# Kernel tuning notes

Measured on AMD Instinct MI355X. Metric: run time of the kernel, lower is better.

The kernel has to match this reference:

```python
import jax, jax.numpy as jnp
import numpy as np

N, D, S, E, H, L = 20000, 256, 4, 320000, 5, 3
EPS = 1e-5


def _layer_norm(x, g, b):
    m = x.mean(-1, keepdims=True)
    v = ((x - m) ** 2).mean(-1, keepdims=True)
    return (x - m) * jax.lax.rsqrt(v + EPS) * g + b


def _gcn_conv(h, src, dst, w, W, b):
    # GCNConv with symmetric normalization and added self-loops (weight 1).
    loops = jnp.arange(N, dtype=src.dtype)
    s = jnp.concatenate([src, loops])
    t = jnp.concatenate([dst, loops])
    we = jnp.concatenate([w, jnp.ones((N,), h.dtype)])
    deg = jax.ops.segment_sum(we, t, num_segments=N)
    dinv = jnp.where(deg > 0, jax.lax.rsqrt(jnp.maximum(deg, EPS)), 0.0)
    norm = dinv[s] * we * dinv[t]          # [E+N]
    hW = h @ W                              # [N, D]
    msg = norm[:, None] * hW[s]             # [E+N, D] gather
    return jax.ops.segment_sum(msg, t, num_segments=N) + b  # scatter-add


def _gelu(x):
    return jax.nn.gelu(x, approximate=False)  # torch nn.GELU default (exact)


def setup_inputs() -> dict:
    key = jax.random.key(0)
    ks = jax.random.split(key, 24)
    f32 = jnp.float32
    w = lambda k, sh, s=0.05: jax.random.normal(k, sh, f32) * s
    inp = {
        "x": jax.random.normal(ks[0], (S, N, D), f32),
        "edge_src": jax.random.randint(ks[1], (E,), 0, N, jnp.int32),
        "edge_dst": jax.random.randint(ks[2], (E,), 0, N, jnp.int32),
        "edge_weight": jax.random.uniform(ks[3], (E,), f32),
        # 3 GCNConv(d, d) layers
        "gcn_W": w(ks[4], (L, D, D)),
        "gcn_b": jnp.zeros((L, D), f32),
        # 3 LayerNorm(d)
        "ln_g": jnp.ones((L, D), f32),
        "ln_b": jnp.zeros((L, D), f32),
        # nn.GRU(d, d) single layer, batch_first
        "gru_Wih": w(ks[5], (3 * D, D)),
        "gru_Whh": w(ks[6], (3 * D, D)),
        "gru_bih": jnp.zeros((3 * D,), f32),
        "gru_bhh": jnp.zeros((3 * D,), f32),
        # ForecastHead: d -> d/2 -> d/4 -> H
        "fc1_W": w(ks[7], (D // 2, D)), "fc1_b": jnp.zeros((D // 2,), f32),
        "fc2_W": w(ks[8], (D // 4, D // 2)), "fc2_b": jnp.zeros((D // 4,), f32),
        "fc3_W": w(ks[9], (H, D // 4)), "fc3_b": jnp.zeros((H,), f32),
        # DirectionHead: d -> d/4 -> H
        "dh1_W": w(ks[10], (D // 4, D)), "dh1_b": jnp.zeros((D // 4,), f32),
        "dh2_W": w(ks[11], (H, D // 4)), "dh2_b": jnp.zeros((H,), f32),
    }
    return inp


def reference(x, edge_src, edge_dst, edge_weight, gcn_W, gcn_b, ln_g, ln_b,
              gru_Wih, gru_Whh, gru_bih, gru_bhh,
              fc1_W, fc1_b, fc2_W, fc2_b, fc3_W, fc3_b,
              dh1_W, dh1_b, dh2_W, dh2_b):
    # Per-snapshot GCN stack (dropout = identity in eval). Loop over the
    # small fixed snapshot count to bound the gather/scatter intermediate.
    feats = []
    for si in range(S):
        h = x[si]
        for l in range(L):
            h = _gcn_conv(h, edge_src, edge_dst, edge_weight, gcn_W[l], gcn_b[l])
            h = _layer_norm(h, ln_g[l], ln_b[l])
            h = jax.nn.relu(h)
        feats.append(h)
    seq = jnp.stack(feats, axis=0)  # [S, N, D] (time-major for scan)

    def gru_step(h, x_t):
        gi = x_t @ gru_Wih.T + gru_bih
        gh = h @ gru_Whh.T + gru_bhh
        ir, iz, ig = jnp.split(gi, 3, axis=-1)
        hr, hz, hg = jnp.split(gh, 3, axis=-1)
        r = jax.nn.sigmoid(ir + hr)
        z = jax.nn.sigmoid(iz + hz)
        n = jnp.tanh(ig + r * hg)
        return (1.0 - z) * n + z * h, None

    h_last, _ = jax.lax.scan(gru_step, jnp.zeros((N, D), x.dtype), seq)

    f = _gelu(h_last @ fc1_W.T + fc1_b)
    f = _gelu(f @ fc2_W.T + fc2_b)
    forecast = f @ fc3_W.T + fc3_b            # [N, H]
    d = _gelu(h_last @ dh1_W.T + dh1_b)
    direction = d @ dh2_W.T + dh2_b           # [N, H]
    return forecast, direction
```

## Files before the change

kernel.cpp:

```cpp
#include <hip/hip_runtime.h>
#include <hip/hip_bf16.h>

constexpr int Nn = 20000;
constexpr int D  = 256;
constexpr int S  = 4;
constexpr int E  = 320000;
constexpr int H  = 5;
constexpr int L  = 3;

using bf16 = __hip_bfloat16;
typedef __attribute__((ext_vector_type(8))) short v8s;
typedef __attribute__((ext_vector_type(4))) float v4f;

#define GLOBAL_AS __attribute__((address_space(1)))
#define LDS_AS    __attribute__((address_space(3)))

__device__ __forceinline__ float gelu_exact(float x) {
    return 0.5f * x * (1.0f + erff(x * 0.70710678118654752440f));
}
__device__ __forceinline__ unsigned short f2bu(float f) {
    bf16 h = __float2bfloat16(f);
    return *reinterpret_cast<unsigned short*>(&h);
}
__device__ __forceinline__ float b2f(unsigned short u) {
    unsigned int v = (unsigned int)u << 16;
    return __uint_as_float(v);
}

__global__ void init_deg_cnt_kernel(float* deg, int* cnt, int n) {
    int i = blockIdx.x * blockDim.x + threadIdx.x;
    if (i < n) { deg[i] = 1.0f; cnt[i] = 0; }
}
__global__ void deg_hist_kernel(const int* __restrict__ dst, const float* __restrict__ w,
                                float* __restrict__ deg, int* __restrict__ cnt, int e) {
    int i = blockIdx.x * blockDim.x + threadIdx.x;
    if (i < e) {
        int d = dst[i];
        atomicAdd(&deg[d], w[i]);
        atomicAdd(&cnt[d], 1);
    }
}
__global__ void dinv_kernel(const float* __restrict__ deg, float* __restrict__ dinv,
                            float* __restrict__ selfnorm, int n) {
    int i = blockIdx.x * blockDim.x + threadIdx.x;
    if (i < n) {
        float dg = deg[i];
        float dv = dg > 0.0f ? rsqrtf(fmaxf(dg, 1e-5f)) : 0.0f;
        dinv[i] = dv;
        selfnorm[i] = dv * dv;
    }
}
__global__ __launch_bounds__(1024) void scan_rowptr_kernel(int* __restrict__ cnt,
                                                           int* __restrict__ rowptr, int n) {
    __shared__ int wsum[16];
    __shared__ int woff[16];
    int t = threadIdx.x;
    int wave = t >> 6, lane = t & 63;
    int chunk = (n + 1023) / 1024;
    int start = t * chunk;
    int end = start + chunk; if (end > n) end = n;
    int s = 0;
    for (int i = start; i < end; ++i) s += cnt[i];
    int incl = s;
#pragma unroll
    for (int off = 1; off < 64; off <<= 1) {
        int v = __shfl_up(incl, off);
        if (lane >= off) incl += v;
    }
    int excl = incl - s;
    if (lane == 63) wsum[wave] = incl;
    __syncthreads();
    if (t == 0) {
        int acc = 0;
        for (int i = 0; i < 16; ++i) { woff[i] = acc; acc += wsum[i]; }
        rowptr[n] = acc;
    }
    __syncthreads();
    int acc = woff[wave] + excl;
    for (int i = start; i < end; ++i) {
        rowptr[i] = acc; acc += cnt[i]; cnt[i] = 0;
    }
}
__global__ void csr_fill_kernel(const int* __restrict__ src, const int* __restrict__ dst,
                                const float* __restrict__ w, const float* __restrict__ dinv,
                                const int* __restrict__ rowptr,
                                int* __restrict__ cursor, int* __restrict__ csrc,
                                float* __restrict__ cnorm, int e) {
    int i = blockIdx.x * blockDim.x + threadIdx.x;
    if (i < e) {
        int sN = src[i], dN = dst[i];
        int pos = rowptr[dN] + atomicAdd(&cursor[dN], 1);
        csrc[pos] = sN;
        cnorm[pos] = dinv[sN] * w[i] * dinv[dN];
    }
}
constexpr int CW0 = L * D * D;
constexpr int CW1 = CW0 + 3 * D * D;
constexpr int CW2 = CW1 + 3 * D * D;
constexpr int CW3 = CW2 + 192 * 256;
constexpr int CW4 = CW3 + 64 * 128;
constexpr int CW5 = CW4 + 4 * D;
constexpr int CW6 = CW5 + 192;
__global__ void convert_weights_kernel(
    const float* __restrict__ gcn_W, const float* __restrict__ Wih,
    const float* __restrict__ Whh, const float* __restrict__ fc1W,
    const float* __restrict__ fc2W, const float* __restrict__ dh1W,
    const float* __restrict__ bih, const float* __restrict__ bhh,
    const float* __restrict__ fc1b, const float* __restrict__ dh1b,
    unsigned short* __restrict__ Wtb, unsigned short* __restrict__ Wihb,
    unsigned short* __restrict__ Whhb, unsigned short* __restrict__ fc1dh1Wb,
    unsigned short* __restrict__ fc2Wb,
    float* __restrict__ gbias, float* __restrict__ hcat)
{
    int i = blockIdx.x * blockDim.x + threadIdx.x;
    if (i < CW0) {
        int l = i / (D * D);
        int rem = i - l * D * D;
        int k = rem / D;
        int n = rem - k * D;
        Wtb[(size_t)l * D * D + (size_t)n * D + k] = f2bu(gcn_W[i]);
    } else if (i < CW1) { int j = i - CW0; Wihb[j] = f2bu(Wih[j]); }
    else if (i < CW2)   { int j = i - CW1; Whhb[j] = f2bu(Whh[j]); }
    else if (i < CW3) {
        int j = i - CW2;
        fc1dh1Wb[j] = (j < 128 * 256) ? f2bu(fc1W[j]) : f2bu(dh1W[j - 128 * 256]);
    }
    else if (i < CW4)   { int j = i - CW3; fc2Wb[j] = f2bu(fc2W[j]); }
    else if (i < CW5) {
        int j = i - CW4;
        int g = j >> 8, d = j & 255;
        float v;
        if (g == 0)      v = bih[d] + bhh[d];
        else if (g == 1) v = bih[D + d] + bhh[D + d];
        else if (g == 2) v = bih[2 * D + d];
        else             v = bhh[2 * D + d];
        gbias[j] = v;
    }
    else if (i < CW6) {
        int j = i - CW5;
        hcat[j] = (j < 128) ? fc1b[j] : dh1b[j - 128];
    }
}

#define GBM 128
#define GBN 128
#define GBK 64
template<int OUT_MODE, int ACT, int XIN>
__global__ __launch_bounds__(256) void gemm_bt_bf16_kernel(
    const unsigned short* __restrict__ A, int lda,
    const unsigned short* __restrict__ B,
    const float* __restrict__ bias, unsigned short* __restrict__ C,
    int M, int N, int K)
{
    __shared__ short As[GBM * GBK];
    __shared__ short Bs[GBN * GBK];
    int tid = threadIdx.x;
    int wave = tid >> 6, lane = tid & 63;
    int ln = lane & 15, quad = lane >> 4;
    int wr = wave >> 1, wc = wave & 1;
    int bm = blockIdx.y * GBM, bn = blockIdx.x * GBN;

    v4f acc[4][4];
#pragma unroll
    for (int i = 0; i < 4; ++i)
#pragma unroll
        for (int j = 0; j < 4; ++j)
            acc[i][j] = (v4f)(0.0f);

    int lrow = lane >> 3;
    int lcol = (lane & 7) * 8;

    for (int k0 = 0; k0 < K; k0 += GBK) {
#pragma unroll
        for (int c = 0; c < 4; ++c) {
            int seg = wave * 4 + c;
            int row = seg * 8 + lrow;
            int gm = bm + row; if (gm >= M) gm = M - 1;
            if (XIN) {
                int xr = (gm & 3) * Nn + (gm >> 2);
                const float* xp = (const float*)A + (size_t)xr * D + k0 + lcol;
                float4 v0 = *(const float4*)xp;
                float4 v1 = *(const float4*)(xp + 4);
                v8s o;
                o[0] = (short)f2bu(v0.x); o[1] = (short)f2bu(v0.y);
                o[2] = (short)f2bu(v0.z); o[3] = (short)f2bu(v0.w);
                o[4] = (short)f2bu(v1.x); o[5] = (short)f2bu(v1.y);
                o[6] = (short)f2bu(v1.z); o[7] = (short)f2bu(v1.w);
                *(v8s*)(&As[row * GBK + lcol]) = o;
            } else {
                __builtin_amdgcn_global_load_lds(
                    (const GLOBAL_AS unsigned int*)(A + (size_t)gm * lda + k0 + lcol),
                    (LDS_AS unsigned int*)(&As[row * GBK + lcol]), 16, 0, 0);
            }
            int gn = bn + row; if (gn >= N) gn = N - 1;
            __builtin_amdgcn_global_load_lds(
                (const GLOBAL_AS unsigned int*)(B + (size_t)gn * K + k0 + lcol),
                (LDS_AS unsigned int*)(&Bs[row * GBK + lcol]), 16, 0, 0);
        }
        __syncthreads();
#pragma unroll
        for (int ks = 0; ks < 2; ++ks) {
            v8s af[4], bfr[4];
#pragma unroll
            for (int i = 0; i < 4; ++i) {
                int row = wr * 64 + i * 16 + ln;
                af[i] = *(const v8s*)(&As[row * GBK + ks * 32 + quad * 8]);
            }
#pragma unroll
            for (int j = 0; j < 4; ++j) {
                int row = wc * 64 + j * 16 + ln;
                bfr[j] = *(const v8s*)(&Bs[row * GBK + ks * 32 + quad * 8]);
            }
#pragma unroll
            for (int i = 0; i < 4; ++i)
#pragma unroll
                for (int j = 0; j < 4; ++j)
                    acc[i][j] = __builtin_amdgcn_mfma_f32_16x16x32_bf16(af[i], bfr[j], acc[i][j], 0, 0, 0);
        }
        __syncthreads();
    }
#pragma unroll
    for (int i = 0; i < 4; ++i) {
        int gmb = bm + wr * 64 + i * 16 + quad * 4;
#pragma unroll
        for (int j = 0; j < 4; ++j) {
            int gn = bn + wc * 64 + j * 16 + ln;
            float bv = (bias && gn < N) ? bias[gn] : 0.0f;
            if (OUT_MODE == 2) {
                ushort4 u;
                u.x = f2bu(acc[i][j][0] + bv);
                u.y = f2bu(acc[i][j][1] + bv);
                u.z = f2bu(acc[i][j][2] + bv);
                u.w = f2bu(acc[i][j][3] + bv);
                int node = gmb >> 2;
                *(ushort4*)(C + ((size_t)node * D + gn) * 4) = u;
            } else {
                if (gn < N) {
#pragma unroll
                    for (int r = 0; r < 4; ++r) {
                        int gm = gmb + r;
                        if (gm < M) {
                            float v = acc[i][j][r] + bv;
                            if (ACT == 1) v = gelu_exact(v);
                            C[(size_t)gm * N + gn] = f2bu(v);
                        }
                    }
                }
            }
        }
    }
}

__global__ __launch_bounds__(256) void gru_fused_kernel(
    const unsigned short* __restrict__ feat, int fstride,
    const unsigned short* __restrict__ hbf,
    const unsigned short* __restrict__ Wihb,
    const unsigned short* __restrict__ Whhb,
    const float* __restrict__ gbias,
    float* __restrict__ h, unsigned short* __restrict__ hb,
    int write_f32, int first)
{
    __shared__ short As[64 * 64];
    __shared__ short Bs[192 * 64];
    int tid = threadIdx.x;
    int wave = tid >> 6, lane = tid & 63;
    int ln = lane & 15, quad = lane >> 4;
    int wm = wave >> 1, wn = wave & 1;
    int bm = blockIdx.y * 64;
    int bn = blockIdx.x * 64;

    v4f accR[2][2], accZ[2][2], accG[2][2], accHG[2][2];
#pragma unroll
    for (int mi = 0; mi < 2; ++mi)
#pragma unroll
        for (int nj = 0; nj < 2; ++nj) {
            accR[mi][nj] = (v4f)(0.0f); accZ[mi][nj] = (v4f)(0.0f);
            accG[mi][nj] = (v4f)(0.0f); accHG[mi][nj] = (v4f)(0.0f);
        }

    int lrow = lane >> 3, lcol = (lane & 7) * 8;
    int nphase = first ? 1 : 2;

    for (int phase = 0; phase < nphase; ++phase) {
        const unsigned short* A = phase ? hbf : feat;
        int astr = phase ? D : fstride;
        const unsigned short* W = phase ? Whhb : Wihb;
        for (int k0 = 0; k0 < D; k0 += 64) {
#pragma unroll
            for (int c = 0; c < 2; ++c) {
                int row = wave * 16 + c * 8 + lrow;
                int gm = bm + row; if (gm >= Nn) gm = Nn - 1;
                __builtin_amdgcn_global_load_lds(
                    (const GLOBAL_AS unsigned int*)(A + (size_t)gm * astr + k0 + lcol),
                    (LDS_AS unsigned int*)(&As[row * 64 + lcol]), 16, 0, 0);
            }
#pragma unroll
            for (int c = 0; c < 6; ++c) {
                int row = wave * 48 + c * 8 + lrow;
                int g = row >> 6, dloc = row & 63;
                __builtin_amdgcn_global_load_lds(
                    (const GLOBAL_AS unsigned int*)(W + ((size_t)(g * D + bn + dloc)) * D + k0 + lcol),
                    (LDS_AS unsigned int*)(&Bs[row * 64 + lcol]), 16, 0, 0);
            }
            __syncthreads();
#pragma unroll
            for (int ks = 0; ks < 2; ++ks) {
                v8s am[2];
#pragma unroll
                for (int mi = 0; mi < 2; ++mi)
                    am[mi] = *(const v8s*)(&As[(wm * 32 + mi * 16 + ln) * 64 + ks * 32 + quad * 8]);
#pragma unroll
                for (int g = 0; g < 3; ++g) {
#pragma unroll
                    for (int nj = 0; nj < 2; ++nj) {
                        v8s bf = *(const v8s*)(&Bs[(g * 64 + wn * 32 + nj * 16 + ln) * 64 + ks * 32 + quad * 8]);
#pragma unroll
                        for (int mi = 0; mi < 2; ++mi) {
                            if (g == 0)
                                accR[mi][nj] = __builtin_amdgcn_mfma_f32_16x16x32_bf16(am[mi], bf, accR[mi][nj], 0, 0, 0);
                            else if (g == 1)
                                accZ[mi][nj] = __builtin_amdgcn_mfma_f32_16x16x32_bf16(am[mi], bf, accZ[mi][nj], 0, 0, 0);
                            else if (phase == 0)
                                accG[mi][nj] = __builtin_amdgcn_mfma_f32_16x16x32_bf16(am[mi], bf, accG[mi][nj], 0, 0, 0);
                            else
                                accHG[mi][nj] = __builtin_amdgcn_mfma_f32_16x16x32_bf16(am[mi], bf, accHG[mi][nj], 0, 0, 0);
                        }
                    }
                }
            }
            __syncthreads();
        }
    }
#pragma unroll
    for (int mi = 0; mi < 2; ++mi) {
        int gm0 = bm + wm * 32 + mi * 16 + quad * 4;
#pragma unroll
        for (int nj = 0; nj < 2; ++nj) {
            int gn = bn + wn * 32 + nj * 16 + ln;
            float vbr = gbias[gn], vbz = gbias[D + gn];
            float vbig = gbias[2 * D + gn], vbhg = gbias[3 * D + gn];
#pragma unroll
            for (int r = 0; r < 4; ++r) {
                int gm = gm0 + r;
                if (gm < Nn) {
                    float rv = 1.0f / (1.0f + expf(-(accR[mi][nj][r] + vbr)));
                    float zv = 1.0f / (1.0f + expf(-(accZ[mi][nj][r] + vbz)));
                    float nv = tanhf(accG[mi][nj][r] + vbig + rv * (accHG[mi][nj][r] + vbhg));
                    float hold = first ? 0.0f : h[(size_t)gm * D + gn];
                    float hv = (1.0f - zv) * nv + zv * hold;
                    if (write_f32) h[(size_t)gm * D + gn] = hv;
                    hb[(size_t)gm * D + gn] = f2bu(hv);
                }
            }
        }
    }
}

__global__ __launch_bounds__(256) void gcn_agg_ln_relu4_kernel(
    const unsigned short* __restrict__ hWb, const int* __restrict__ rowptr,
    const int* __restrict__ csrc, const float* __restrict__ cnorm,
    const float* __restrict__ selfnorm,
    const float* __restrict__ gcn_b, const float* __restrict__ ln_g,
    const float* __restrict__ ln_b, unsigned short* __restrict__ out)
{
    int wave = threadIdx.x >> 6, lane = threadIdx.x & 63;
    int i = blockIdx.x * 4 + wave;
    const ushort4* tbl = (const ushort4*)hWb;

    float acc[4][4];
    {
        float w = selfnorm[i];
#pragma unroll
        for (int q = 0; q < 4; ++q) {
            ushort4 u = tbl[(size_t)i * D + lane + q * 64];
            acc[q][0] = w * b2f(u.x); acc[q][1] = w * b2f(u.y);
            acc[q][2] = w * b2f(u.z); acc[q][3] = w * b2f(u.w);
        }
    }
    int beg = rowptr[i], end = rowptr[i + 1];
    int p = beg;
    for (; p + 1 < end; p += 2) {
        int sA = csrc[p], sB = csrc[p + 1];
        float wA = cnorm[p], wB = cnorm[p + 1];
        ushort4 uA[4], uB[4];
#pragma unroll
        for (int q = 0; q < 4; ++q) uA[q] = tbl[(size_t)sA * D + lane + q * 64];
#pragma unroll
        for (int q = 0; q < 4; ++q) uB[q] = tbl[(size_t)sB * D + lane + q * 64];
#pragma unroll
        for (int q = 0; q < 4; ++q) {
            acc[q][0] = fmaf(wA, b2f(uA[q].x), acc[q][0]);
            acc[q][1] = fmaf(wA, b2f(uA[q].y), acc[q][1]);
            acc[q][2] = fmaf(wA, b2f(uA[q].z), acc[q][2]);
            acc[q][3] = fmaf(wA, b2f(uA[q].w), acc[q][3]);
            acc[q][0] = fmaf(wB, b2f(uB[q].x), acc[q][0]);
            acc[q][1] = fmaf(wB, b2f(uB[q].y), acc[q][1]);
            acc[q][2] = fmaf(wB, b2f(uB[q].z), acc[q][2]);
            acc[q][3] = fmaf(wB, b2f(uB[q].w), acc[q][3]);
        }
    }
    if (p < end) {
        int sA = csrc[p]; float wA = cnorm[p];
#pragma unroll
        for (int q = 0; q < 4; ++q) {
            ushort4 u = tbl[(size_t)sA * D + lane + q * 64];
            acc[q][0] = fmaf(wA, b2f(u.x), acc[q][0]);
            acc[q][1] = fmaf(wA, b2f(u.y), acc[q][1]);
            acc[q][2] = fmaf(wA, b2f(u.z), acc[q][2]);
            acc[q][3] = fmaf(wA, b2f(u.w), acc[q][3]);
        }
    }
#pragma unroll
    for (int q = 0; q < 4; ++q) {
        float bb = gcn_b[lane + q * 64];
        acc[q][0] += bb; acc[q][1] += bb; acc[q][2] += bb; acc[q][3] += bb;
    }
    float s1[4], s2[4];
#pragma unroll
    for (int s = 0; s < 4; ++s) {
        s1[s] = acc[0][s] + acc[1][s] + acc[2][s] + acc[3][s];
        s2[s] = acc[0][s] * acc[0][s] + acc[1][s] * acc[1][s]
              + acc[2][s] * acc[2][s] + acc[3][s] * acc[3][s];
    }
#pragma unroll
    for (int off = 32; off > 0; off >>= 1) {
#pragma unroll
        for (int s = 0; s < 4; ++s) {
            s1[s] += __shfl_xor(s1[s], off);
            s2[s] += __shfl_xor(s2[s], off);
        }
    }
    const float inv = 1.0f / D;
    float m[4], rr[4];
#pragma unroll
    for (int s = 0; s < 4; ++s) {
        m[s] = s1[s] * inv;
        rr[s] = rsqrtf(s2[s] * inv - m[s] * m[s] + 1e-5f);
    }
    size_t ob = (size_t)(i << 2) * D;
#pragma unroll
    for (int q = 0; q < 4; ++q) {
        int d = lane + q * 64;
        float g = ln_g[d], lb = ln_b[d];
#pragma unroll
        for (int s = 0; s < 4; ++s) {
            float y = (acc[q][s] - m[s]) * rr[s] * g + lb;
            out[ob + (size_t)s * D + d] = f2bu(fmaxf(y, 0.0f));
        }
    }
}

__global__ void head5_bf_kernel(const unsigned short* __restrict__ A, int lda,
                                const float* __restrict__ W,
                                const float* __restrict__ b, float* __restrict__ C,
                                int M, int K) {
    int idx = blockIdx.x * blockDim.x + threadIdx.x;
    if (idx >= M * H) return;
    int m = idx / H;
    int h = idx - m * H;
    const ushort4* ar = (const ushort4*)(A + (size_t)m * lda);
    const float* wr = W + (size_t)h * K;
    float s = 0.0f;
    for (int k4 = 0; k4 < K / 4; ++k4) {
        ushort4 u = ar[k4];
        s = fmaf(b2f(u.x), wr[4 * k4 + 0], s);
        s = fmaf(b2f(u.y), wr[4 * k4 + 1], s);
        s = fmaf(b2f(u.z), wr[4 * k4 + 2], s);
        s = fmaf(b2f(u.w), wr[4 * k4 + 3], s);
    }
    C[idx] = s + b[h];
}

extern "C" void kernel_launch(void* const* d_in, const int* in_sizes, int n_in,
                              void* d_out, int out_size, void* d_ws, size_t ws_size,
                              hipStream_t stream)
{
    const float* x     = (const float*)d_in[0];
    const int*   esrc  = (const int*)d_in[1];
    const int*   edst  = (const int*)d_in[2];
    const float* ew    = (const float*)d_in[3];
    const float* gcn_W = (const float*)d_in[4];
    const float* gcn_b = (const float*)d_in[5];
    const float* ln_g  = (const float*)d_in[6];
    const float* ln_b  = (const float*)d_in[7];
    const float* Wih   = (const float*)d_in[8];
    const float* Whh   = (const float*)d_in[9];
    const float* bih   = (const float*)d_in[10];
    const float* bhh   = (const float*)d_in[11];
    const float* fc1W  = (const float*)d_in[12];
    const float* fc1b  = (const float*)d_in[13];
    const float* fc2W  = (const float*)d_in[14];
    const float* fc2b  = (const float*)d_in[15];
    const float* fc3W  = (const float*)d_in[16];
    const float* fc3b  = (const float*)d_in[17];
    const float* dh1W  = (const float*)d_in[18];
    const float* dh1b  = (const float*)d_in[19];
    const float* dh2W  = (const float*)d_in[20];
    const float* dh2b  = (const float*)d_in[21];

    float* out = (float*)d_out;

    char* p = (char*)d_ws;
    auto alloc = [&](size_t bytes) -> void* {
        void* r = (void*)p;
        p += (bytes + 255) & ~(size_t)255;
        return r;
    };
    float* deg      = (float*)alloc((size_t)Nn * 4);
    float* dinv     = (float*)alloc((size_t)Nn * 4);
    float* selfnorm = (float*)alloc((size_t)Nn * 4);
    int*   rowptr   = (int*)alloc((size_t)(Nn + 1) * 4);
    int*   cnt      = (int*)alloc((size_t)Nn * 4);
    int*   csrc     = (int*)alloc((size_t)E * 4);
    float* cnorm    = (float*)alloc((size_t)E * 4);
    unsigned short* Wtb      = (unsigned short*)alloc((size_t)L * D * D * 2);
    unsigned short* Wihb     = (unsigned short*)alloc((size_t)3 * D * D * 2);
    unsigned short* Whhb     = (unsigned short*)alloc((size_t)3 * D * D * 2);
    unsigned short* fc1dh1Wb = (unsigned short*)alloc((size_t)192 * 256 * 2);
    unsigned short* fc2Wb    = (unsigned short*)alloc((size_t)64 * 128 * 2);
    float* gbias    = (float*)alloc((size_t)4 * D * 4);
    float* hcat     = (float*)alloc((size_t)192 * 4);
    unsigned short* bufA  = (unsigned short*)alloc((size_t)Nn * S * D * 2);
    unsigned short* hWb   = (unsigned short*)alloc((size_t)Nn * D * S * 2);
    float* hgru     = (float*)alloc((size_t)Nn * D * 4);
    unsigned short* hgru_bf = (unsigned short*)alloc((size_t)Nn * D * 2);
    unsigned short* f1cat = (unsigned short*)alloc((size_t)Nn * 192 * 2);
    unsigned short* f2    = (unsigned short*)alloc((size_t)Nn * 64 * 2);

    auto cdiv = [](int a, int b) { return (a + b - 1) / b; };

    init_deg_cnt_kernel<<<cdiv(Nn, 256), 256, 0, stream>>>(deg, cnt, Nn);
    deg_hist_kernel<<<cdiv(E, 256), 256, 0, stream>>>(edst, ew, deg, cnt, E);
    dinv_kernel<<<cdiv(Nn, 256), 256, 0, stream>>>(deg, dinv, selfnorm, Nn);
    scan_rowptr_kernel<<<1, 1024, 0, stream>>>(cnt, rowptr, Nn);
    csr_fill_kernel<<<cdiv(E, 256), 256, 0, stream>>>(esrc, edst, ew, dinv, rowptr, cnt, csrc, cnorm, E);
    convert_weights_kernel<<<cdiv(CW6, 256), 256, 0, stream>>>(
        gcn_W, Wih, Whh, fc1W, fc2W, dh1W, bih, bhh, fc1b, dh1b,
        Wtb, Wihb, Whhb, fc1dh1Wb, fc2Wb, gbias, hcat);

    {
        dim3 g1(D / GBN, (Nn * S) / GBM);
        gemm_bt_bf16_kernel<2, 0, 1><<<g1, 256, 0, stream>>>(
            (const unsigned short*)x, D, Wtb, nullptr, hWb, Nn * S, D, D);
        gcn_agg_ln_relu4_kernel<<<Nn / 4, 256, 0, stream>>>(
            hWb, rowptr, csrc, cnorm, selfnorm,
            gcn_b, ln_g, ln_b, bufA);
        for (int l = 1; l < L; ++l) {
            gemm_bt_bf16_kernel<2, 0, 0><<<g1, 256, 0, stream>>>(
                bufA, D, Wtb + (size_t)l * D * D, nullptr, hWb, Nn * S, D, D);
            gcn_agg_ln_relu4_kernel<<<Nn / 4, 256, 0, stream>>>(
                hWb, rowptr, csrc, cnorm, selfnorm,
                gcn_b + (size_t)l * D, ln_g + (size_t)l * D, ln_b + (size_t)l * D, bufA);
        }
    }

    for (int s = 0; s < S; ++s) {
        dim3 g2(D / 64, cdiv(Nn, 64));
        gru_fused_kernel<<<g2, 256, 0, stream>>>(
            bufA + (size_t)s * D, S * D, hgru_bf, Wihb, Whhb, gbias,
            hgru, hgru_bf, (s < S - 1) ? 1 : 0, (s == 0) ? 1 : 0);
    }

    {
        dim3 gf1(2, cdiv(Nn, GBM));
        gemm_bt_bf16_kernel<1, 1, 0><<<gf1, 256, 0, stream>>>(
            hgru_bf, D, fc1dh1Wb, hcat, f1cat, Nn, 192, 256);
        dim3 gf2(1, cdiv(Nn, GBM));
        gemm_bt_bf16_kernel<1, 1, 0><<<gf2, 256, 0, stream>>>(
            f1cat, 192, fc2Wb, fc2b, f2, Nn, 64, 128);
        head5_bf_kernel<<<cdiv(Nn * H, 256), 256, 0, stream>>>(f2, 64, fc3W, fc3b, out, Nn, 64);
        head5_bf_kernel<<<cdiv(Nn * H, 256), 256, 0, stream>>>(f1cat + 128, 192, dh2W, dh2b,
                                                               out + (size_t)Nn * H, Nn, 64);
    }
}
```

Measured before the change: 845.7 us.

## Quantize GCN hW table to int8 with per-row-quarter scales for gather

The GEMM epilogue now quantizes hW for each node to int8, with one fp32 scale per 64-column quarter across the 4 snapshots. It writes a packed int8 table and a scale array. The aggregation kernel gathers 4-byte words instead of 8-byte bf16 vectors and dequantizes with the folded edge-norm times scale. This halves the bytes in the gather that dominates aggregation, at the cost of int8 precision loss, which may exceed the tolerance.

```diff
diff --git a/kernel.cpp b/kernel.cpp
--- a/kernel.cpp
+++ b/kernel.cpp
@@ -26,6 +26,10 @@
     unsigned int v = (unsigned int)u << 16;
     return __uint_as_float(v);
 }
+__device__ __forceinline__ float sx0(unsigned int v) { return (float)((int)(v << 24) >> 24); }
+__device__ __forceinline__ float sx1(unsigned int v) { return (float)((int)(v << 16) >> 24); }
+__device__ __forceinline__ float sx2(unsigned int v) { return (float)((int)(v << 8) >> 24); }
+__device__ __forceinline__ float sx3(unsigned int v) { return (float)((int)v >> 24); }
 
 __global__ void init_deg_cnt_kernel(float* deg, int* cnt, int n) {
     int i = blockIdx.x * blockDim.x + threadIdx.x;
@@ -150,6 +154,7 @@
     const unsigned short* __restrict__ A, int lda,
     const unsigned short* __restrict__ B,
     const float* __restrict__ bias, unsigned short* __restrict__ C,
+    float* __restrict__ Cscale,
     int M, int N, int K)
 {
     __shared__ short As[GBM * GBK];
@@ -219,22 +224,46 @@
         }
         __syncthreads();
     }
-#pragma unroll
-    for (int i = 0; i < 4; ++i) {
-        int gmb = bm + wr * 64 + i * 16 + quad * 4;
-#pragma unroll
-        for (int j = 0; j < 4; ++j) {
-            int gn = bn + wc * 64 + j * 16 + ln;
-            float bv = (bias && gn < N) ? bias[gn] : 0.0f;
-            if (OUT_MODE == 2) {
-                ushort4 u;
-                u.x = f2bu(acc[i][j][0] + bv);
-                u.y = f2bu(acc[i][j][1] + bv);
-                u.z = f2bu(acc[i][j][2] + bv);
-                u.w = f2bu(acc[i][j][3] + bv);
-                int node = gmb >> 2;
-                *(ushort4*)(C + ((size_t)node * D + gn) * 4) = u;
-            } else {
+    if (OUT_MODE == 3) {
+#pragma unroll
+        for (int i = 0; i < 4; ++i) {
+            int gmb = bm + wr * 64 + i * 16 + quad * 4;
+            int node = gmb >> 2;
+            float mx = 0.0f;
+#pragma unroll
+            for (int j = 0; j < 4; ++j)
+#pragma unroll
+                for (int r = 0; r < 4; ++r)
+                    mx = fmaxf(mx, fabsf(acc[i][j][r]));
+            mx = fmaxf(mx, __shfl_xor(mx, 1));
+            mx = fmaxf(mx, __shfl_xor(mx, 2));
+            mx = fmaxf(mx, __shfl_xor(mx, 4));
+            mx = fmaxf(mx, __shfl_xor(mx, 8));
+            float inv = mx > 0.0f ? 127.0f / mx : 0.0f;
+#pragma unroll
+            for (int j = 0; j < 4; ++j) {
+                int gn = bn + wc * 64 + j * 16 + ln;
+                int q0 = (int)lrintf(fminf(fmaxf(acc[i][j][0] * inv, -127.0f), 127.0f));
+                int q1 = (int)lrintf(fminf(fmaxf(acc[i][j][1] * inv, -127.0f), 127.0f));
+                int q2 = (int)lrintf(fminf(fmaxf(acc[i][j][2] * inv, -127.0f), 127.0f));
+                int q3 = (int)lrintf(fminf(fmaxf(acc[i][j][3] * inv, -127.0f), 127.0f));
+                unsigned int pk = (q0 & 0xff) | ((q1 & 0xff) << 8)
+                                | ((q2 & 0xff) << 16) | ((q3 & 0xff) << 24);
+                ((unsigned int*)C)[(size_t)node * D + gn] = pk;
+            }
+            if (ln == 0) {
+                int quarter = (bn >> 6) + wc;
+                Cscale[(size_t)node * 4 + quarter] = mx * (1.0f / 127.0f);
+            }
+        }
+    } else {
+#pragma unroll
+        for (int i = 0; i < 4; ++i) {
+            int gmb = bm + wr * 64 + i * 16 + quad * 4;
+#pragma unroll
+            for (int j = 0; j < 4; ++j) {
+                int gn = bn + wc * 64 + j * 16 + ln;
+                float bv = (bias && gn < N) ? bias[gn] : 0.0f;
                 if (gn < N) {
 #pragma unroll
                     for (int r = 0; r < 4; ++r) {
@@ -357,7 +386,8 @@
 }
 
 __global__ __launch_bounds__(256) void gcn_agg_ln_relu4_kernel(
-    const unsigned short* __restrict__ hWb, const int* __restrict__ rowptr,
+    const unsigned int* __restrict__ tbl8, const float4* __restrict__ scales,
+    const int* __restrict__ rowptr,
     const int* __restrict__ csrc, const float* __restrict__ cnorm,
     const float* __restrict__ selfnorm,
     const float* __restrict__ gcn_b, const float* __restrict__ ln_g,
@@ -365,16 +395,17 @@
 {
     int wave = threadIdx.x >> 6, lane = threadIdx.x & 63;
     int i = blockIdx.x * 4 + wave;
-    const ushort4* tbl = (const ushort4*)hWb;
 
     float acc[4][4];
     {
         float w = selfnorm[i];
+        float4 sc = scales[i];
+        float wq[4] = {w * sc.x, w * sc.y, w * sc.z, w * sc.w};
 #pragma unroll
         for (int q = 0; q < 4; ++q) {
-            ushort4 u = tbl[(size_t)i * D + lane + q * 64];
-            acc[q][0] = w * b2f(u.x); acc[q][1] = w * b2f(u.y);
-            acc[q][2] = w * b2f(u.z); acc[q][3] = w * b2f(u.w);
+            unsigned int v = tbl8[(size_t)i * D + lane + q * 64];
+            acc[q][0] = wq[q] * sx0(v); acc[q][1] = wq[q] * sx1(v);
+            acc[q][2] = wq[q] * sx2(v); acc[q][3] = wq[q] * sx3(v);
         }
     }
     int beg = rowptr[i], end = rowptr[i + 1];
@@ -382,32 +413,38 @@
     for (; p + 1 < end; p += 2) {
         int sA = csrc[p], sB = csrc[p + 1];
         float wA = cnorm[p], wB = cnorm[p + 1];
-        ushort4 uA[4], uB[4];
-#pragma unroll
-        for (int q = 0; q < 4; ++q) uA[q] = tbl[(size_t)sA * D + lane + q * 64];
-#pragma unroll
-        for (int q = 0; q < 4; ++q) uB[q] = tbl[(size_t)sB * D + lane + q * 64];
+        float4 scA = scales[sA], scB = scales[sB];
+        unsigned int uA[4], uB[4];
 #pragma unroll
         for (int q = 0; q < 4; ++q) {
-            acc[q][0] = fmaf(wA, b2f(uA[q].x), acc[q][0]);
-            acc[q][1] = fmaf(wA, b2f(uA[q].y), acc[q][1]);
-            acc[q][2] = fmaf(wA, b2f(uA[q].z), acc[q][2]);
-            acc[q][3] = fmaf(wA, b2f(uA[q].w), acc[q][3]);
-            acc[q][0] = fmaf(wB, b2f(uB[q].x), acc[q][0]);
-            acc[q][1] = fmaf(wB, b2f(uB[q].y), acc[q][1]);
-            acc[q][2] = fmaf(wB, b2f(uB[q].z), acc[q][2]);
-            acc[q][3] = fmaf(wB, b2f(uB[q].w), acc[q][3]);
+            uA[q] = tbl8[(size_t)sA * D + lane + q * 64];
+            uB[q] = tbl8[(size_t)sB * D + lane + q * 64];
+        }
+        float wqA[4] = {wA * scA.x, wA * scA.y, wA * scA.z, wA * scA.w};
+        float wqB[4] = {wB * scB.x, wB * scB.y, wB * scB.z, wB * scB.w};
+#pragma unroll
+        for (int q = 0; q < 4; ++q) {
+            acc[q][0] = fmaf(wqA[q], sx0(uA[q]), acc[q][0]);
+            acc[q][1] = fmaf(wqA[q], sx1(uA[q]), acc[q][1]);
+            acc[q][2] = fmaf(wqA[q], sx2(uA[q]), acc[q][2]);
+            acc[q][3] = fmaf(wqA[q], sx3(uA[q]), acc[q][3]);
+            acc[q][0] = fmaf(wqB[q], sx0(uB[q]), acc[q][0]);
+            acc[q][1] = fmaf(wqB[q], sx1(uB[q]), acc[q][1]);
+            acc[q][2] = fmaf(wqB[q], sx2(uB[q]), acc[q][2]);
+            acc[q][3] = fmaf(wqB[q], sx3(uB[q]), acc[q][3]);
         }
     }
     if (p < end) {
         int sA = csrc[p]; float wA = cnorm[p];
+        float4 scA = scales[sA];
+        float wqA[4] = {wA * scA.x, wA * scA.y, wA * scA.z, wA * scA.w};
 #pragma unroll
         for (int q = 0; q < 4; ++q) {
-            ushort4 u = tbl[(size_t)sA * D + lane + q * 64];
-            acc[q][0] = fmaf(wA, b2f(u.x), acc[q][0]);
-            acc[q][1] = fmaf(wA, b2f(u.y), acc[q][1]);
-            acc[q][2] = fmaf(wA, b2f(u.z), acc[q][2]);
-            acc[q][3] = fmaf(wA, b2f(u.w), acc[q][3]);
+            unsigned int v = tbl8[(size_t)sA * D + lane + q * 64];
+            acc[q][0] = fmaf(wqA[q], sx0(v), acc[q][0]);
+            acc[q][1] = fmaf(wqA[q], sx1(v), acc[q][1]);
+            acc[q][2] = fmaf(wqA[q], sx2(v), acc[q][2]);
+            acc[q][3] = fmaf(wqA[q], sx3(v), acc[q][3]);
         }
     }
 #pragma unroll
@@ -521,7 +558,8 @@
     float* gbias    = (float*)alloc((size_t)4 * D * 4);
     float* hcat     = (float*)alloc((size_t)192 * 4);
     unsigned short* bufA  = (unsigned short*)alloc((size_t)Nn * S * D * 2);
-    unsigned short* hWb   = (unsigned short*)alloc((size_t)Nn * D * S * 2);
+    unsigned int*   tbl8  = (unsigned int*)alloc((size_t)Nn * D * 4);
+    float*          tscal = (float*)alloc((size_t)Nn * 4 * 4);
     float* hgru     = (float*)alloc((size_t)Nn * D * 4);
     unsigned short* hgru_bf = (unsigned short*)alloc((size_t)Nn * D * 2);
     unsigned short* f1cat = (unsigned short*)alloc((size_t)Nn * 192 * 2);
@@ -540,16 +578,18 @@
 
     {
         dim3 g1(D / GBN, (Nn * S) / GBM);
-        gemm_bt_bf16_kernel<2, 0, 1><<<g1, 256, 0, stream>>>(
-            (const unsigned short*)x, D, Wtb, nullptr, hWb, Nn * S, D, D);
+        gemm_bt_bf16_kernel<3, 0, 1><<<g1, 256, 0, stream>>>(
+            (const unsigned short*)x, D, Wtb, nullptr, (unsigned short*)tbl8, tscal,
+            Nn * S, D, D);
         gcn_agg_ln_relu4_kernel<<<Nn / 4, 256, 0, stream>>>(
-            hWb, rowptr, csrc, cnorm, selfnorm,
+            tbl8, (const float4*)tscal, rowptr, csrc, cnorm, selfnorm,
             gcn_b, ln_g, ln_b, bufA);
         for (int l = 1; l < L; ++l) {
-            gemm_bt_bf16_kernel<2, 0, 0><<<g1, 256, 0, stream>>>(
-                bufA, D, Wtb + (size_t)l * D * D, nullptr, hWb, Nn * S, D, D);
+            gemm_bt_bf16_kernel<3, 0, 0><<<g1, 256, 0, stream>>>(
+                bufA, D, Wtb + (size_t)l * D * D, nullptr, (unsigned short*)tbl8, tscal,
+                Nn * S, D, D);
             gcn_agg_ln_relu4_kernel<<<Nn / 4, 256, 0, stream>>>(
-                hWb, rowptr, csrc, cnorm, selfnorm,
+                tbl8, (const float4*)tscal, rowptr, csrc, cnorm, selfnorm,
                 gcn_b + (size_t)l * D, ln_g + (size_t)l * D, ln_b + (size_t)l * D, bufA);
         }
     }
@@ -564,10 +604,10 @@
     {
         dim3 gf1(2, cdiv(Nn, GBM));
         gemm_bt_bf16_kernel<1, 1, 0><<<gf1, 256, 0, stream>>>(
-            hgru_bf, D, fc1dh1Wb, hcat, f1cat, Nn, 192, 256);
+            hgru_bf, D, fc1dh1Wb, hcat, f1cat, nullptr, Nn, 192, 256);
         dim3 gf2(1, cdiv(Nn, GBM));
         gemm_bt_bf16_kernel<1, 1, 0><<<gf2, 256, 0, stream>>>(
-            f1cat, 192, fc2Wb, fc2b, f2, Nn, 64, 128);
+            f1cat, 192, fc2Wb, fc2b, f2, nullptr, Nn, 64, 128);
         head5_bf_kernel<<<cdiv(Nn * H, 256), 256, 0, stream>>>(f2, 64, fc3W, fc3b, out, Nn, 64);
         head5_bf_kernel<<<cdiv(Nn * H, 256), 256, 0, stream>>>(f1cat + 128, 192, dh2W, dh2b,
                                                                out + (size_t)Nn * H, Nn, 64);
```

Result: faster. 713.8 us (-15.6%).
